# Optimization experiments

Hardware: AMD Instinct MI355X
Metric: run time of the kernel (lower is better)

## Reference

```python
import jax, jax.numpy as jnp
import numpy as np

N_NODES = 50000
N_EDGES = 800000
IN_F, HID, N_CLS = 128, 128, 40


def gcn_conv(x, row, col, ew, W, b, n):
    # PyG GCNConv with add_self_loops=True, normalize=True (gcn_norm):
    # out = D^{-1/2} (A + I) D^{-1/2} (x W) + b, aggregation at target = col.
    h = x @ W                                        # [N, F_out]
    loop = jnp.arange(n)
    row_f = jnp.concatenate([row, loop])             # self-loop weight = 1
    col_f = jnp.concatenate([col, loop])
    ew_f = jnp.concatenate([ew, jnp.ones((n,), dtype=ew.dtype)])
    deg = jax.ops.segment_sum(ew_f, col_f, num_segments=n)
    dinv = jnp.where(deg > 0, jax.lax.rsqrt(deg), 0.0)
    norm = dinv[row_f] * ew_f * dinv[col_f]          # [E+N]
    msg = norm[:, None] * h[row_f]                   # gather + scale
    out = jax.ops.segment_sum(msg, col_f, num_segments=n)  # scatter-add
    return out + b


def setup_inputs() -> dict:
    key = jax.random.key(0)
    ks = jax.random.split(key, 8)
    glorot = lambda k, fi, fo: jax.random.normal(k, (fi, fo), jnp.float32) * np.sqrt(2.0 / (fi + fo))
    return {
        "x": jax.random.normal(ks[0], (N_NODES, IN_F), jnp.float32),
        "edge_weight": jax.random.uniform(ks[1], (N_EDGES,), jnp.float32),
        "W1": glorot(ks[2], IN_F, HID),
        "b1": jnp.zeros((HID,), jnp.float32),
        "W2": glorot(ks[3], HID, HID),
        "b2": jnp.zeros((HID,), jnp.float32),
        "W3": glorot(ks[4], HID, N_CLS),
        "b3": jnp.zeros((N_CLS,), jnp.float32),
        "edge_index": jax.random.randint(ks[5], (2, N_EDGES), 0, N_NODES, jnp.int64),
        "target_mask": jnp.ones((N_NODES,), jnp.bool_),
    }


def reference(x, edge_weight, W1, b1, W2, b2, W3, b3, edge_index, target_mask):
    n = x.shape[0]
    row, col = edge_index[0], edge_index[1]
    h = gcn_conv(x, row, col, edge_weight, W1, b1, n)
    h = jax.nn.relu(h)  # dropout is identity in eval mode
    h = gcn_conv(h, row, col, edge_weight, W2, b2, n)
    h = jax.nn.relu(h)
    h = gcn_conv(h, row, col, edge_weight, W3, b3, n)
    return h[target_mask]
```

## Files before the change

### kernel.cpp

```cpp
#include <hip/hip_runtime.h>
#include <hip/hip_fp16.h>

#define N_NODES 50000
#define N_EDGES 800000
#define HID 128
#define N_CLS 40
#define CAP 64
#define TILES32 1563
#define CNT_BLOCKS 3125
#define NODE_WAVES 12500

static inline int cdiv(int a, int b) { return (a + b - 1) / b; }

__device__ __forceinline__ void fill_body(int e, const int* __restrict__ row,
                                          const int* __restrict__ col,
                                          const float* __restrict__ ew,
                                          int* __restrict__ cnt,
                                          uint2* __restrict__ bkt) {
    if (e < N_EDGES) {
        int c = col[e];
        int pos = atomicAdd(&cnt[c], 1);
        if (pos < CAP)
            bkt[(size_t)c * CAP + pos] = make_uint2((unsigned)row[e],
                                                    __float_as_uint(ew[e]));
    }
}

__device__ __forceinline__ void gemm128_body(int b, const float* __restrict__ X,
                                             const float* __restrict__ W,
                                             __half* __restrict__ out) {
    __shared__ float xsT[128][36];
    __shared__ float wch[32][128];
    const int t = threadIdx.x;
    const int row0 = b * 32;

    #pragma unroll
    for (int i = 0; i < 4; ++i) {
        int idx = t + i * 256;
        int row = idx >> 5;
        int k4  = idx & 31;
        float4 v = make_float4(0.f, 0.f, 0.f, 0.f);
        if (row0 + row < N_NODES)
            v = *(const float4*)&X[(size_t)(row0 + row) * 128 + k4 * 4];
        xsT[k4 * 4 + 0][row] = v.x;
        xsT[k4 * 4 + 1][row] = v.y;
        xsT[k4 * 4 + 2][row] = v.z;
        xsT[k4 * 4 + 3][row] = v.w;
    }

    const int c0 = (t & 31) * 4;
    const int r0 = (t >> 5) * 4;
    float acc[4][4];
    #pragma unroll
    for (int i = 0; i < 4; ++i)
        #pragma unroll
        for (int j = 0; j < 4; ++j) acc[i][j] = 0.f;

    for (int kk = 0; kk < 128; kk += 32) {
        __syncthreads();
        #pragma unroll
        for (int i = 0; i < 4; ++i) {
            int idx = t + i * 256;
            int wr = idx >> 5;
            int wc4 = idx & 31;
            *(float4*)&wch[wr][wc4 * 4] =
                *(const float4*)&W[(size_t)(kk + wr) * 128 + wc4 * 4];
        }
        __syncthreads();
        #pragma unroll 4
        for (int k = 0; k < 32; ++k) {
            float4 a = *(const float4*)&xsT[kk + k][r0];
            float4 w = *(const float4*)&wch[k][c0];
            acc[0][0] = fmaf(a.x, w.x, acc[0][0]);
            acc[0][1] = fmaf(a.x, w.y, acc[0][1]);
            acc[0][2] = fmaf(a.x, w.z, acc[0][2]);
            acc[0][3] = fmaf(a.x, w.w, acc[0][3]);
            acc[1][0] = fmaf(a.y, w.x, acc[1][0]);
            acc[1][1] = fmaf(a.y, w.y, acc[1][1]);
            acc[1][2] = fmaf(a.y, w.z, acc[1][2]);
            acc[1][3] = fmaf(a.y, w.w, acc[1][3]);
            acc[2][0] = fmaf(a.z, w.x, acc[2][0]);
            acc[2][1] = fmaf(a.z, w.y, acc[2][1]);
            acc[2][2] = fmaf(a.z, w.z, acc[2][2]);
            acc[2][3] = fmaf(a.z, w.w, acc[2][3]);
            acc[3][0] = fmaf(a.w, w.x, acc[3][0]);
            acc[3][1] = fmaf(a.w, w.y, acc[3][1]);
            acc[3][2] = fmaf(a.w, w.z, acc[3][2]);
            acc[3][3] = fmaf(a.w, w.w, acc[3][3]);
        }
    }

    #pragma unroll
    for (int i = 0; i < 4; ++i) {
        int r = row0 + r0 + i;
        if (r < N_NODES) {
            union { __half2 h2[2]; float2 f2; } u;
            u.h2[0] = __floats2half2_rn(acc[i][0], acc[i][1]);
            u.h2[1] = __floats2half2_rn(acc[i][2], acc[i][3]);
            *(float2*)&out[(size_t)r * 128 + c0] = u.f2;
        }
    }
}

__global__ __launch_bounds__(256) void fused_gemm1_fill(
    const float* __restrict__ X, const float* __restrict__ W, __half* __restrict__ out,
    const int* __restrict__ row, const int* __restrict__ col,
    const float* __restrict__ ew, int* __restrict__ cnt, uint2* __restrict__ bkt) {
    int id = blockIdx.x;
    if (id & 1) {
        fill_body((id >> 1) * 256 + threadIdx.x, row, col, ew, cnt, bkt);
    } else {
        int b = id >> 1;
        if (b < TILES32) gemm128_body(b, X, W, out);
    }
}

__global__ __launch_bounds__(256) void dinv_kernel(
    const int* __restrict__ cnt, const uint2* __restrict__ bkt,
    float* __restrict__ dinv) {
    int node = blockIdx.x * 4 + (threadIdx.x >> 6);
    int lane = threadIdx.x & 63;
    if (node >= N_NODES) return;
    int n = min(cnt[node], CAP);
    float ewv = 0.f;
    if (lane < n) ewv = __uint_as_float(bkt[(size_t)node * CAP + lane].y);
    #pragma unroll
    for (int off = 32; off > 0; off >>= 1)
        ewv += __shfl_down(ewv, off);
    if (lane == 0) dinv[node] = rsqrtf(ewv + 1.0f);
}

__device__ __forceinline__ void fma_h8(float w, uint4 g, float* acc) {
    float2 a0 = __half22float2(*(const __half2*)&g.x);
    float2 a1 = __half22float2(*(const __half2*)&g.y);
    float2 a2 = __half22float2(*(const __half2*)&g.z);
    float2 a3 = __half22float2(*(const __half2*)&g.w);
    acc[0] = fmaf(w, a0.x, acc[0]);
    acc[1] = fmaf(w, a0.y, acc[1]);
    acc[2] = fmaf(w, a1.x, acc[2]);
    acc[3] = fmaf(w, a1.y, acc[3]);
    acc[4] = fmaf(w, a2.x, acc[4]);
    acc[5] = fmaf(w, a2.y, acc[5]);
    acc[6] = fmaf(w, a3.x, acc[6]);
    acc[7] = fmaf(w, a3.y, acc[7]);
}

__device__ __forceinline__ void agg128_node16(int node, int sl,
                                              const int* __restrict__ cnt,
                                              const uint2* __restrict__ bkt,
                                              const __half* __restrict__ h,
                                              const float* __restrict__ dinv,
                                              const float* __restrict__ bias,
                                              float* acc) {
    #pragma unroll
    for (int j = 0; j < 8; ++j) acc[j] = 0.f;
    if (node >= N_NODES) return;
    int f = sl * 8;
    int beg = node * CAP;
    int end = beg + min(cnt[node], CAP);
    float dn = dinv[node];
    int k = beg;
    for (; k + 8 <= end; k += 8) {
        uint2 e0 = bkt[k],   e1 = bkt[k+1], e2 = bkt[k+2], e3 = bkt[k+3];
        uint2 e4 = bkt[k+4], e5 = bkt[k+5], e6 = bkt[k+6], e7 = bkt[k+7];
        uint4 g0 = *(const uint4*)&h[(size_t)e0.x * 128 + f];
        uint4 g1 = *(const uint4*)&h[(size_t)e1.x * 128 + f];
        uint4 g2 = *(const uint4*)&h[(size_t)e2.x * 128 + f];
        uint4 g3 = *(const uint4*)&h[(size_t)e3.x * 128 + f];
        uint4 g4 = *(const uint4*)&h[(size_t)e4.x * 128 + f];
        uint4 g5 = *(const uint4*)&h[(size_t)e5.x * 128 + f];
        uint4 g6 = *(const uint4*)&h[(size_t)e6.x * 128 + f];
        uint4 g7 = *(const uint4*)&h[(size_t)e7.x * 128 + f];
        float w0 = dinv[e0.x] * __uint_as_float(e0.y) * dn;
        float w1 = dinv[e1.x] * __uint_as_float(e1.y) * dn;
        float w2 = dinv[e2.x] * __uint_as_float(e2.y) * dn;
        float w3 = dinv[e3.x] * __uint_as_float(e3.y) * dn;
        float w4 = dinv[e4.x] * __uint_as_float(e4.y) * dn;
        float w5 = dinv[e5.x] * __uint_as_float(e5.y) * dn;
        float w6 = dinv[e6.x] * __uint_as_float(e6.y) * dn;
        float w7 = dinv[e7.x] * __uint_as_float(e7.y) * dn;
        fma_h8(w0, g0, acc);
        fma_h8(w1, g1, acc);
        fma_h8(w2, g2, acc);
        fma_h8(w3, g3, acc);
        fma_h8(w4, g4, acc);
        fma_h8(w5, g5, acc);
        fma_h8(w6, g6, acc);
        fma_h8(w7, g7, acc);
    }
    for (; k + 4 <= end; k += 4) {
        uint2 e0 = bkt[k], e1 = bkt[k+1], e2 = bkt[k+2], e3 = bkt[k+3];
        uint4 g0 = *(const uint4*)&h[(size_t)e0.x * 128 + f];
        uint4 g1 = *(const uint4*)&h[(size_t)e1.x * 128 + f];
        uint4 g2 = *(const uint4*)&h[(size_t)e2.x * 128 + f];
        uint4 g3 = *(const uint4*)&h[(size_t)e3.x * 128 + f];
        float w0 = dinv[e0.x] * __uint_as_float(e0.y) * dn;
        float w1 = dinv[e1.x] * __uint_as_float(e1.y) * dn;
        float w2 = dinv[e2.x] * __uint_as_float(e2.y) * dn;
        float w3 = dinv[e3.x] * __uint_as_float(e3.y) * dn;
        fma_h8(w0, g0, acc);
        fma_h8(w1, g1, acc);
        fma_h8(w2, g2, acc);
        fma_h8(w3, g3, acc);
    }
    for (; k < end; ++k) {
        uint2 e = bkt[k];
        uint4 g = *(const uint4*)&h[(size_t)e.x * 128 + f];
        float w = dinv[e.x] * __uint_as_float(e.y) * dn;
        fma_h8(w, g, acc);
    }
    uint4 gs = *(const uint4*)&h[(size_t)node * 128 + f];
    fma_h8(dn * dn, gs, acc);
    float4 b0 = *(const float4*)&bias[f];
    float4 b1 = *(const float4*)&bias[f + 4];
    acc[0] = fmaxf(acc[0] + b0.x, 0.f);
    acc[1] = fmaxf(acc[1] + b0.y, 0.f);
    acc[2] = fmaxf(acc[2] + b0.z, 0.f);
    acc[3] = fmaxf(acc[3] + b0.w, 0.f);
    acc[4] = fmaxf(acc[4] + b1.x, 0.f);
    acc[5] = fmaxf(acc[5] + b1.y, 0.f);
    acc[6] = fmaxf(acc[6] + b1.z, 0.f);
    acc[7] = fmaxf(acc[7] + b1.w, 0.f);
}

__device__ __forceinline__ void agg_tile_to_lds(int row0, const int* cnt,
                                                const uint2* bkt, const __half* h,
                                                const float* dinv, const float* bias,
                                                float (*xsT)[36]) {
    int wave = threadIdx.x >> 6;
    int lane = threadIdx.x & 63;
    int sub  = lane >> 4;
    int sl   = lane & 15;
    int f = sl * 8;
    #pragma unroll
    for (int i = 0; i < 2; ++i) {
        int r = i * 16 + wave * 4 + sub;
        float acc[8];
        agg128_node16(row0 + r, sl, cnt, bkt, h, dinv, bias, acc);
        #pragma unroll
        for (int j = 0; j < 8; ++j)
            xsT[f + j][r] = acc[j];
    }
}

__global__ __launch_bounds__(256) void agg_gemm128_kernel(
    const int* __restrict__ cnt, const uint2* __restrict__ bkt,
    const __half* __restrict__ h, const float* __restrict__ dinv,
    const float* __restrict__ bias, const float* __restrict__ W,
    __half* __restrict__ out) {
    __shared__ float xsT[128][36];
    __shared__ float wch[32][128];
    const int t = threadIdx.x;
    const int row0 = blockIdx.x * 32;

    agg_tile_to_lds(row0, cnt, bkt, h, dinv, bias, xsT);

    const int c0 = (t & 31) * 4;
    const int r0 = (t >> 5) * 4;
    float acc[4][4];
    #pragma unroll
    for (int i = 0; i < 4; ++i)
        #pragma unroll
        for (int j = 0; j < 4; ++j) acc[i][j] = 0.f;

    for (int kk = 0; kk < 128; kk += 32) {
        __syncthreads();
        #pragma unroll
        for (int i = 0; i < 4; ++i) {
            int idx = t + i * 256;
            int wr = idx >> 5;
            int wc4 = idx & 31;
            *(float4*)&wch[wr][wc4 * 4] =
                *(const float4*)&W[(size_t)(kk + wr) * 128 + wc4 * 4];
        }
        __syncthreads();
        #pragma unroll 4
        for (int k = 0; k < 32; ++k) {
            float4 a = *(const float4*)&xsT[kk + k][r0];
            float4 w = *(const float4*)&wch[k][c0];
            acc[0][0] = fmaf(a.x, w.x, acc[0][0]);
            acc[0][1] = fmaf(a.x, w.y, acc[0][1]);
            acc[0][2] = fmaf(a.x, w.z, acc[0][2]);
            acc[0][3] = fmaf(a.x, w.w, acc[0][3]);
            acc[1][0] = fmaf(a.y, w.x, acc[1][0]);
            acc[1][1] = fmaf(a.y, w.y, acc[1][1]);
            acc[1][2] = fmaf(a.y, w.z, acc[1][2]);
            acc[1][3] = fmaf(a.y, w.w, acc[1][3]);
            acc[2][0] = fmaf(a.z, w.x, acc[2][0]);
            acc[2][1] = fmaf(a.z, w.y, acc[2][1]);
            acc[2][2] = fmaf(a.z, w.z, acc[2][2]);
            acc[2][3] = fmaf(a.z, w.w, acc[2][3]);
            acc[3][0] = fmaf(a.w, w.x, acc[3][0]);
            acc[3][1] = fmaf(a.w, w.y, acc[3][1]);
            acc[3][2] = fmaf(a.w, w.z, acc[3][2]);
            acc[3][3] = fmaf(a.w, w.w, acc[3][3]);
        }
    }

    #pragma unroll
    for (int i = 0; i < 4; ++i) {
        int r = row0 + r0 + i;
        if (r < N_NODES) {
            union { __half2 h2[2]; float2 f2; } u;
            u.h2[0] = __floats2half2_rn(acc[i][0], acc[i][1]);
            u.h2[1] = __floats2half2_rn(acc[i][2], acc[i][3]);
            *(float2*)&out[(size_t)r * 128 + c0] = u.f2;
        }
    }
}

__global__ __launch_bounds__(256) void agg_gemm40_kernel(
    const int* __restrict__ cnt, const uint2* __restrict__ bkt,
    const __half* __restrict__ h, const float* __restrict__ dinv,
    const float* __restrict__ bias, const float* __restrict__ W3,
    __half* __restrict__ out) {
    __shared__ float xsT[128][36];
    const int row0 = blockIdx.x * 32;
    agg_tile_to_lds(row0, cnt, bkt, h, dinv, bias, xsT);
    __syncthreads();
    for (int idx = threadIdx.x; idx < 32 * N_CLS; idx += 256) {
        int r = idx / N_CLS;
        int c = idx % N_CLS;
        float acc = 0.f;
        #pragma unroll 8
        for (int k = 0; k < 128; ++k)
            acc = fmaf(xsT[k][r], W3[k * N_CLS + c], acc);
        int node = row0 + r;
        if (node < N_NODES)
            out[(size_t)node * 64 + c] = __float2half(acc);
    }
}

__global__ __launch_bounds__(256) void agg40_kernel(
    const int* __restrict__ cnt, const uint2* __restrict__ bkt,
    const __half* __restrict__ h, const float* __restrict__ dinv,
    const float* __restrict__ b, float* __restrict__ out) {
    int wave = threadIdx.x >> 6;
    int lane = threadIdx.x & 63;
    int node = blockIdx.x * 4 + wave;
    if (node >= N_NODES || lane >= N_CLS) return;
    int beg = node * CAP;
    int end = beg + min(cnt[node], CAP);
    float dn = dinv[node];
    float acc = 0.f;
    int k = beg;
    for (; k + 4 <= end; k += 4) {
        uint2 e0 = bkt[k], e1 = bkt[k+1], e2 = bkt[k+2], e3 = bkt[k+3];
        float g0 = __half2float(h[(size_t)e0.x * 64 + lane]);
        float g1 = __half2float(h[(size_t)e1.x * 64 + lane]);
        float g2 = __half2float(h[(size_t)e2.x * 64 + lane]);
        float g3 = __half2float(h[(size_t)e3.x * 64 + lane]);
        float w0 = dinv[e0.x] * __uint_as_float(e0.y) * dn;
        float w1 = dinv[e1.x] * __uint_as_float(e1.y) * dn;
        float w2 = dinv[e2.x] * __uint_as_float(e2.y) * dn;
        float w3 = dinv[e3.x] * __uint_as_float(e3.y) * dn;
        acc = fmaf(w0, g0, acc);
        acc = fmaf(w1, g1, acc);
        acc = fmaf(w2, g2, acc);
        acc = fmaf(w3, g3, acc);
    }
    for (; k < end; ++k) {
        uint2 e = bkt[k];
        float w = dinv[e.x] * __uint_as_float(e.y) * dn;
        acc = fmaf(w, __half2float(h[(size_t)e.x * 64 + lane]), acc);
    }
    acc = fmaf(dn * dn, __half2float(h[(size_t)node * 64 + lane]), acc) + b[lane];
    out[(size_t)node * N_CLS + lane] = acc;
}

extern "C" void kernel_launch(void* const* d_in, const int* in_sizes, int n_in,
                              void* d_out, int out_size, void* d_ws, size_t ws_size,
                              hipStream_t stream) {
    const float* x  = (const float*)d_in[0];
    const float* ew = (const float*)d_in[1];
    const float* W1 = (const float*)d_in[2];
    const float* b1 = (const float*)d_in[3];
    const float* W2 = (const float*)d_in[4];
    const float* b2 = (const float*)d_in[5];
    const float* W3 = (const float*)d_in[6];
    const float* b3 = (const float*)d_in[7];
    const int*   ei = (const int*)d_in[8];
    const int* row = ei;
    const int* col = ei + N_EDGES;
    float* out = (float*)d_out;

    char* ws = (char*)d_ws;
    size_t off = 0;
    auto alloc = [&](size_t bytes) -> void* {
        void* p = (void*)(ws + off);
        off = (off + bytes + 255) & ~(size_t)255;
        return p;
    };
    int*    cnt  = (int*)alloc((size_t)N_NODES * 4);
    float*  dinv = (float*)alloc((size_t)N_NODES * 4);
    uint2*  bkt  = (uint2*)alloc((size_t)N_NODES * CAP * 8);
    __half* h16a = (__half*)alloc((size_t)N_NODES * HID * 2);
    __half* h16b = (__half*)alloc((size_t)N_NODES * HID * 2);
    __half* h40  = (__half*)alloc((size_t)N_NODES * 64 * 2);

    hipMemsetAsync(cnt, 0, (size_t)N_NODES * 4, stream);

    fused_gemm1_fill<<<2 * CNT_BLOCKS, 256, 0, stream>>>(x, W1, h16a, row, col, ew, cnt, bkt);
    dinv_kernel<<<NODE_WAVES, 256, 0, stream>>>(cnt, bkt, dinv);
    agg_gemm128_kernel<<<TILES32, 256, 0, stream>>>(cnt, bkt, h16a, dinv, b1, W2, h16b);
    agg_gemm40_kernel<<<TILES32, 256, 0, stream>>>(cnt, bkt, h16b, dinv, b2, W3, h40);
    agg40_kernel<<<cdiv(N_NODES, 4), 256, 0, stream>>>(cnt, bkt, h40, dinv, b3, out);
}
```

Before: 304.5 us.

## Pack degree sum and count into one 64-bit atomic, drop dinv kernel

The fill step now atomically adds a packed 64-bit value holding the edge count in the high bits and a fixed-point weighted degree in the low 44 bits. This removes the separate dinv reduction kernel and its launch, and the aggregation kernels recompute rsqrt from the packed value on the fly. The trade-offs are 8-byte instead of 4-byte per-neighbor degree loads, an extra rsqrt per edge, and fixed-point rounding of the degree sum. The W2 staging chunk in the agg_gemm128 kernel is also halved to 16 rows, which cuts shared memory but doubles the number of sync steps.

```diff
diff --git a/kernel.cpp b/kernel.cpp
--- a/kernel.cpp
+++ b/kernel.cpp
@@ -8,21 +8,32 @@
 #define CAP 64
 #define TILES32 1563
 #define CNT_BLOCKS 3125
-#define NODE_WAVES 12500
+#define DEG_SCALE 2097152.0f
+#define DEG_MASK ((1ull << 44) - 1)
 
 static inline int cdiv(int a, int b) { return (a + b - 1) / b; }
+
+__device__ __forceinline__ float pdinv(unsigned long long p) {
+    return rsqrtf((float)(p & DEG_MASK) * (1.0f / DEG_SCALE) + 1.0f);
+}
+__device__ __forceinline__ int pcnt(unsigned long long p) {
+    return (int)(p >> 44);
+}
 
 __device__ __forceinline__ void fill_body(int e, const int* __restrict__ row,
                                           const int* __restrict__ col,
                                           const float* __restrict__ ew,
-                                          int* __restrict__ cnt,
+                                          unsigned long long* __restrict__ packed,
                                           uint2* __restrict__ bkt) {
     if (e < N_EDGES) {
         int c = col[e];
-        int pos = atomicAdd(&cnt[c], 1);
+        float w = ew[e];
+        unsigned long long v =
+            (1ull << 44) | (unsigned long long)__float2uint_rn(w * DEG_SCALE);
+        unsigned long long old = atomicAdd(&packed[c], v);
+        int pos = pcnt(old);
         if (pos < CAP)
-            bkt[(size_t)c * CAP + pos] = make_uint2((unsigned)row[e],
-                                                    __float_as_uint(ew[e]));
+            bkt[(size_t)c * CAP + pos] = make_uint2((unsigned)row[e], __float_as_uint(w));
     }
 }
 
@@ -105,29 +116,15 @@
 __global__ __launch_bounds__(256) void fused_gemm1_fill(
     const float* __restrict__ X, const float* __restrict__ W, __half* __restrict__ out,
     const int* __restrict__ row, const int* __restrict__ col,
-    const float* __restrict__ ew, int* __restrict__ cnt, uint2* __restrict__ bkt) {
+    const float* __restrict__ ew, unsigned long long* __restrict__ packed,
+    uint2* __restrict__ bkt) {
     int id = blockIdx.x;
     if (id & 1) {
-        fill_body((id >> 1) * 256 + threadIdx.x, row, col, ew, cnt, bkt);
+        fill_body((id >> 1) * 256 + threadIdx.x, row, col, ew, packed, bkt);
     } else {
         int b = id >> 1;
         if (b < TILES32) gemm128_body(b, X, W, out);
     }
-}
-
-__global__ __launch_bounds__(256) void dinv_kernel(
-    const int* __restrict__ cnt, const uint2* __restrict__ bkt,
-    float* __restrict__ dinv) {
-    int node = blockIdx.x * 4 + (threadIdx.x >> 6);
-    int lane = threadIdx.x & 63;
-    if (node >= N_NODES) return;
-    int n = min(cnt[node], CAP);
-    float ewv = 0.f;
-    if (lane < n) ewv = __uint_as_float(bkt[(size_t)node * CAP + lane].y);
-    #pragma unroll
-    for (int off = 32; off > 0; off >>= 1)
-        ewv += __shfl_down(ewv, off);
-    if (lane == 0) dinv[node] = rsqrtf(ewv + 1.0f);
 }
 
 __device__ __forceinline__ void fma_h8(float w, uint4 g, float* acc) {
@@ -146,19 +143,19 @@
 }
 
 __device__ __forceinline__ void agg128_node16(int node, int sl,
-                                              const int* __restrict__ cnt,
+                                              const unsigned long long* __restrict__ packed,
                                               const uint2* __restrict__ bkt,
                                               const __half* __restrict__ h,
-                                              const float* __restrict__ dinv,
                                               const float* __restrict__ bias,
                                               float* acc) {
     #pragma unroll
     for (int j = 0; j < 8; ++j) acc[j] = 0.f;
     if (node >= N_NODES) return;
     int f = sl * 8;
+    unsigned long long pn = packed[node];
+    float dn = pdinv(pn);
     int beg = node * CAP;
-    int end = beg + min(cnt[node], CAP);
-    float dn = dinv[node];
+    int end = beg + min(pcnt(pn), CAP);
     int k = beg;
     for (; k + 8 <= end; k += 8) {
         uint2 e0 = bkt[k],   e1 = bkt[k+1], e2 = bkt[k+2], e3 = bkt[k+3];
@@ -171,14 +168,14 @@
         uint4 g5 = *(const uint4*)&h[(size_t)e5.x * 128 + f];
         uint4 g6 = *(const uint4*)&h[(size_t)e6.x * 128 + f];
         uint4 g7 = *(const uint4*)&h[(size_t)e7.x * 128 + f];
-        float w0 = dinv[e0.x] * __uint_as_float(e0.y) * dn;
-        float w1 = dinv[e1.x] * __uint_as_float(e1.y) * dn;
-        float w2 = dinv[e2.x] * __uint_as_float(e2.y) * dn;
-        float w3 = dinv[e3.x] * __uint_as_float(e3.y) * dn;
-        float w4 = dinv[e4.x] * __uint_as_float(e4.y) * dn;
-        float w5 = dinv[e5.x] * __uint_as_float(e5.y) * dn;
-        float w6 = dinv[e6.x] * __uint_as_float(e6.y) * dn;
-        float w7 = dinv[e7.x] * __uint_as_float(e7.y) * dn;
+        float w0 = pdinv(packed[e0.x]) * __uint_as_float(e0.y) * dn;
+        float w1 = pdinv(packed[e1.x]) * __uint_as_float(e1.y) * dn;
+        float w2 = pdinv(packed[e2.x]) * __uint_as_float(e2.y) * dn;
+        float w3 = pdinv(packed[e3.x]) * __uint_as_float(e3.y) * dn;
+        float w4 = pdinv(packed[e4.x]) * __uint_as_float(e4.y) * dn;
+        float w5 = pdinv(packed[e5.x]) * __uint_as_float(e5.y) * dn;
+        float w6 = pdinv(packed[e6.x]) * __uint_as_float(e6.y) * dn;
+        float w7 = pdinv(packed[e7.x]) * __uint_as_float(e7.y) * dn;
         fma_h8(w0, g0, acc);
         fma_h8(w1, g1, acc);
         fma_h8(w2, g2, acc);
@@ -194,10 +191,10 @@
         uint4 g1 = *(const uint4*)&h[(size_t)e1.x * 128 + f];
         uint4 g2 = *(const uint4*)&h[(size_t)e2.x * 128 + f];
         uint4 g3 = *(const uint4*)&h[(size_t)e3.x * 128 + f];
-        float w0 = dinv[e0.x] * __uint_as_float(e0.y) * dn;
-        float w1 = dinv[e1.x] * __uint_as_float(e1.y) * dn;
-        float w2 = dinv[e2.x] * __uint_as_float(e2.y) * dn;
-        float w3 = dinv[e3.x] * __uint_as_float(e3.y) * dn;
+        float w0 = pdinv(packed[e0.x]) * __uint_as_float(e0.y) * dn;
+        float w1 = pdinv(packed[e1.x]) * __uint_as_float(e1.y) * dn;
+        float w2 = pdinv(packed[e2.x]) * __uint_as_float(e2.y) * dn;
+        float w3 = pdinv(packed[e3.x]) * __uint_as_float(e3.y) * dn;
         fma_h8(w0, g0, acc);
         fma_h8(w1, g1, acc);
         fma_h8(w2, g2, acc);
@@ -206,7 +203,7 @@
     for (; k < end; ++k) {
         uint2 e = bkt[k];
         uint4 g = *(const uint4*)&h[(size_t)e.x * 128 + f];
-        float w = dinv[e.x] * __uint_as_float(e.y) * dn;
+        float w = pdinv(packed[e.x]) * __uint_as_float(e.y) * dn;
         fma_h8(w, g, acc);
     }
     uint4 gs = *(const uint4*)&h[(size_t)node * 128 + f];
@@ -223,10 +220,10 @@
     acc[7] = fmaxf(acc[7] + b1.w, 0.f);
 }
 
-__device__ __forceinline__ void agg_tile_to_lds(int row0, const int* cnt,
+__device__ __forceinline__ void agg_tile_to_lds(int row0,
+                                                const unsigned long long* packed,
                                                 const uint2* bkt, const __half* h,
-                                                const float* dinv, const float* bias,
-                                                float (*xsT)[36]) {
+                                                const float* bias, float (*xsT)[36]) {
     int wave = threadIdx.x >> 6;
     int lane = threadIdx.x & 63;
     int sub  = lane >> 4;
@@ -236,7 +233,7 @@
     for (int i = 0; i < 2; ++i) {
         int r = i * 16 + wave * 4 + sub;
         float acc[8];
-        agg128_node16(row0 + r, sl, cnt, bkt, h, dinv, bias, acc);
+        agg128_node16(row0 + r, sl, packed, bkt, h, bias, acc);
         #pragma unroll
         for (int j = 0; j < 8; ++j)
             xsT[f + j][r] = acc[j];
@@ -244,16 +241,15 @@
 }
 
 __global__ __launch_bounds__(256) void agg_gemm128_kernel(
-    const int* __restrict__ cnt, const uint2* __restrict__ bkt,
-    const __half* __restrict__ h, const float* __restrict__ dinv,
-    const float* __restrict__ bias, const float* __restrict__ W,
-    __half* __restrict__ out) {
+    const unsigned long long* __restrict__ packed, const uint2* __restrict__ bkt,
+    const __half* __restrict__ h, const float* __restrict__ bias,
+    const float* __restrict__ W, __half* __restrict__ out) {
     __shared__ float xsT[128][36];
-    __shared__ float wch[32][128];
+    __shared__ float wch[16][128];
     const int t = threadIdx.x;
     const int row0 = blockIdx.x * 32;
 
-    agg_tile_to_lds(row0, cnt, bkt, h, dinv, bias, xsT);
+    agg_tile_to_lds(row0, packed, bkt, h, bias, xsT);
 
     const int c0 = (t & 31) * 4;
     const int r0 = (t >> 5) * 4;
@@ -263,10 +259,10 @@
         #pragma unroll
         for (int j = 0; j < 4; ++j) acc[i][j] = 0.f;
 
-    for (int kk = 0; kk < 128; kk += 32) {
+    for (int kk = 0; kk < 128; kk += 16) {
         __syncthreads();
         #pragma unroll
-        for (int i = 0; i < 4; ++i) {
+        for (int i = 0; i < 2; ++i) {
             int idx = t + i * 256;
             int wr = idx >> 5;
             int wc4 = idx & 31;
@@ -275,7 +271,7 @@
         }
         __syncthreads();
         #pragma unroll 4
-        for (int k = 0; k < 32; ++k) {
+        for (int k = 0; k < 16; ++k) {
             float4 a = *(const float4*)&xsT[kk + k][r0];
             float4 w = *(const float4*)&wch[k][c0];
             acc[0][0] = fmaf(a.x, w.x, acc[0][0]);
@@ -310,13 +306,12 @@
 }
 
 __global__ __launch_bounds__(256) void agg_gemm40_kernel(
-    const int* __restrict__ cnt, const uint2* __restrict__ bkt,
-    const __half* __restrict__ h, const float* __restrict__ dinv,
-    const float* __restrict__ bias, const float* __restrict__ W3,
-    __half* __restrict__ out) {
+    const unsigned long long* __restrict__ packed, const uint2* __restrict__ bkt,
+    const __half* __restrict__ h, const float* __restrict__ bias,
+    const float* __restrict__ W3, __half* __restrict__ out) {
     __shared__ float xsT[128][36];
     const int row0 = blockIdx.x * 32;
-    agg_tile_to_lds(row0, cnt, bkt, h, dinv, bias, xsT);
+    agg_tile_to_lds(row0, packed, bkt, h, bias, xsT);
     __syncthreads();
     for (int idx = threadIdx.x; idx < 32 * N_CLS; idx += 256) {
         int r = idx / N_CLS;
@@ -332,16 +327,17 @@
 }
 
 __global__ __launch_bounds__(256) void agg40_kernel(
-    const int* __restrict__ cnt, const uint2* __restrict__ bkt,
-    const __half* __restrict__ h, const float* __restrict__ dinv,
-    const float* __restrict__ b, float* __restrict__ out) {
+    const unsigned long long* __restrict__ packed, const uint2* __restrict__ bkt,
+    const __half* __restrict__ h, const float* __restrict__ b,
+    float* __restrict__ out) {
     int wave = threadIdx.x >> 6;
     int lane = threadIdx.x & 63;
     int node = blockIdx.x * 4 + wave;
     if (node >= N_NODES || lane >= N_CLS) return;
+    unsigned long long pn = packed[node];
+    float dn = pdinv(pn);
     int beg = node * CAP;
-    int end = beg + min(cnt[node], CAP);
-    float dn = dinv[node];
+    int end = beg + min(pcnt(pn), CAP);
     float acc = 0.f;
     int k = beg;
     for (; k + 4 <= end; k += 4) {
@@ -350,10 +346,10 @@
         float g1 = __half2float(h[(size_t)e1.x * 64 + lane]);
         float g2 = __half2float(h[(size_t)e2.x * 64 + lane]);
         float g3 = __half2float(h[(size_t)e3.x * 64 + lane]);
-        float w0 = dinv[e0.x] * __uint_as_float(e0.y) * dn;
-        float w1 = dinv[e1.x] * __uint_as_float(e1.y) * dn;
-        float w2 = dinv[e2.x] * __uint_as_float(e2.y) * dn;
-        float w3 = dinv[e3.x] * __uint_as_float(e3.y) * dn;
+        float w0 = pdinv(packed[e0.x]) * __uint_as_float(e0.y) * dn;
+        float w1 = pdinv(packed[e1.x]) * __uint_as_float(e1.y) * dn;
+        float w2 = pdinv(packed[e2.x]) * __uint_as_float(e2.y) * dn;
+        float w3 = pdinv(packed[e3.x]) * __uint_as_float(e3.y) * dn;
         acc = fmaf(w0, g0, acc);
         acc = fmaf(w1, g1, acc);
         acc = fmaf(w2, g2, acc);
@@ -361,7 +357,7 @@
     }
     for (; k < end; ++k) {
         uint2 e = bkt[k];
-        float w = dinv[e.x] * __uint_as_float(e.y) * dn;
+        float w = pdinv(packed[e.x]) * __uint_as_float(e.y) * dn;
         acc = fmaf(w, __half2float(h[(size_t)e.x * 64 + lane]), acc);
     }
     acc = fmaf(dn * dn, __half2float(h[(size_t)node * 64 + lane]), acc) + b[lane];
@@ -391,18 +387,17 @@
         off = (off + bytes + 255) & ~(size_t)255;
         return p;
     };
-    int*    cnt  = (int*)alloc((size_t)N_NODES * 4);
-    float*  dinv = (float*)alloc((size_t)N_NODES * 4);
+    unsigned long long* packed = (unsigned long long*)alloc((size_t)N_NODES * 8);
     uint2*  bkt  = (uint2*)alloc((size_t)N_NODES * CAP * 8);
     __half* h16a = (__half*)alloc((size_t)N_NODES * HID * 2);
     __half* h16b = (__half*)alloc((size_t)N_NODES * HID * 2);
     __half* h40  = (__half*)alloc((size_t)N_NODES * 64 * 2);
 
-    hipMemsetAsync(cnt, 0, (size_t)N_NODES * 4, stream);
-
-    fused_gemm1_fill<<<2 * CNT_BLOCKS, 256, 0, stream>>>(x, W1, h16a, row, col, ew, cnt, bkt);
-    dinv_kernel<<<NODE_WAVES, 256, 0, stream>>>(cnt, bkt, dinv);
-    agg_gemm128_kernel<<<TILES32, 256, 0, stream>>>(cnt, bkt, h16a, dinv, b1, W2, h16b);
-    agg_gemm40_kernel<<<TILES32, 256, 0, stream>>>(cnt, bkt, h16b, dinv, b2, W3, h40);
-    agg40_kernel<<<cdiv(N_NODES, 4), 256, 0, stream>>>(cnt, bkt, h40, dinv, b3, out);
-}
+    hipMemsetAsync(packed, 0, (size_t)N_NODES * 8, stream);
+
+    fused_gemm1_fill<<<2 * CNT_BLOCKS, 256, 0, stream>>>(x, W1, h16a, row, col, ew,
+                                                         packed, bkt);
+    agg_gemm128_kernel<<<TILES32, 256, 0, stream>>>(packed, bkt, h16a, b1, W2, h16b);
+    agg_gemm40_kernel<<<TILES32, 256, 0, stream>>>(packed, bkt, h16b, b2, W3, h40);
+    agg40_kernel<<<cdiv(N_NODES, 4), 256, 0, stream>>>(packed, bkt, h40, b3, out);
+}
```

Result: slower. 321.6 us (+5.6%).

## Pack edge count and fixed-point degree into one 64-bit atomic

Applied to the files above, without the earlier changes.

The fill pass now uses a single 64-bit atomic per edge that adds both the count (upper bits) and a fixed-point edge weight (lower 44 bits). This lets the degree-normalization kernel become a trivial per-node elementwise pass instead of a wave-per-node reduction over the buckets. The W chunk in the agg_gemm128 kernel is also cut from 32 to 16 rows, which lowers LDS use and may raise occupancy but adds more syncs. The fixed-point degree adds a small quantization error, and 64-bit atomics may cost more than 32-bit ones.

```diff
diff --git a/kernel.cpp b/kernel.cpp
--- a/kernel.cpp
+++ b/kernel.cpp
@@ -8,21 +8,30 @@
 #define CAP 64
 #define TILES32 1563
 #define CNT_BLOCKS 3125
-#define NODE_WAVES 12500
+#define DINV_BLOCKS 196
+#define DEG_SCALE 2097152.0f
+#define DEG_MASK ((1ull << 44) - 1)
 
 static inline int cdiv(int a, int b) { return (a + b - 1) / b; }
+
+__device__ __forceinline__ int pcnt(unsigned long long p) {
+    return (int)(p >> 44);
+}
 
 __device__ __forceinline__ void fill_body(int e, const int* __restrict__ row,
                                           const int* __restrict__ col,
                                           const float* __restrict__ ew,
-                                          int* __restrict__ cnt,
+                                          unsigned long long* __restrict__ packed,
                                           uint2* __restrict__ bkt) {
     if (e < N_EDGES) {
         int c = col[e];
-        int pos = atomicAdd(&cnt[c], 1);
+        float w = ew[e];
+        unsigned long long v =
+            (1ull << 44) | (unsigned long long)__float2uint_rn(w * DEG_SCALE);
+        unsigned long long old = atomicAdd(&packed[c], v);
+        int pos = pcnt(old);
         if (pos < CAP)
-            bkt[(size_t)c * CAP + pos] = make_uint2((unsigned)row[e],
-                                                    __float_as_uint(ew[e]));
+            bkt[(size_t)c * CAP + pos] = make_uint2((unsigned)row[e], __float_as_uint(w));
     }
 }
 
@@ -105,29 +114,22 @@
 __global__ __launch_bounds__(256) void fused_gemm1_fill(
     const float* __restrict__ X, const float* __restrict__ W, __half* __restrict__ out,
     const int* __restrict__ row, const int* __restrict__ col,
-    const float* __restrict__ ew, int* __restrict__ cnt, uint2* __restrict__ bkt) {
+    const float* __restrict__ ew, unsigned long long* __restrict__ packed,
+    uint2* __restrict__ bkt) {
     int id = blockIdx.x;
     if (id & 1) {
-        fill_body((id >> 1) * 256 + threadIdx.x, row, col, ew, cnt, bkt);
+        fill_body((id >> 1) * 256 + threadIdx.x, row, col, ew, packed, bkt);
     } else {
         int b = id >> 1;
         if (b < TILES32) gemm128_body(b, X, W, out);
     }
 }
 
-__global__ __launch_bounds__(256) void dinv_kernel(
-    const int* __restrict__ cnt, const uint2* __restrict__ bkt,
-    float* __restrict__ dinv) {
-    int node = blockIdx.x * 4 + (threadIdx.x >> 6);
-    int lane = threadIdx.x & 63;
-    if (node >= N_NODES) return;
-    int n = min(cnt[node], CAP);
-    float ewv = 0.f;
-    if (lane < n) ewv = __uint_as_float(bkt[(size_t)node * CAP + lane].y);
-    #pragma unroll
-    for (int off = 32; off > 0; off >>= 1)
-        ewv += __shfl_down(ewv, off);
-    if (lane == 0) dinv[node] = rsqrtf(ewv + 1.0f);
+__global__ __launch_bounds__(256) void dinv_from_packed(
+    const unsigned long long* __restrict__ packed, float* __restrict__ dinv) {
+    int i = blockIdx.x * 256 + threadIdx.x;
+    if (i < N_NODES)
+        dinv[i] = rsqrtf((float)(packed[i] & DEG_MASK) * (1.0f / DEG_SCALE) + 1.0f);
 }
 
 __device__ __forceinline__ void fma_h8(float w, uint4 g, float* acc) {
@@ -146,7 +148,7 @@
 }
 
 __device__ __forceinline__ void agg128_node16(int node, int sl,
-                                              const int* __restrict__ cnt,
+                                              const unsigned long long* __restrict__ packed,
                                               const uint2* __restrict__ bkt,
                                               const __half* __restrict__ h,
                                               const float* __restrict__ dinv,
@@ -156,9 +158,9 @@
     for (int j = 0; j < 8; ++j) acc[j] = 0.f;
     if (node >= N_NODES) return;
     int f = sl * 8;
+    float dn = dinv[node];
     int beg = node * CAP;
-    int end = beg + min(cnt[node], CAP);
-    float dn = dinv[node];
+    int end = beg + min(pcnt(packed[node]), CAP);
     int k = beg;
     for (; k + 8 <= end; k += 8) {
         uint2 e0 = bkt[k],   e1 = bkt[k+1], e2 = bkt[k+2], e3 = bkt[k+3];
@@ -223,7 +225,8 @@
     acc[7] = fmaxf(acc[7] + b1.w, 0.f);
 }
 
-__device__ __forceinline__ void agg_tile_to_lds(int row0, const int* cnt,
+__device__ __forceinline__ void agg_tile_to_lds(int row0,
+                                                const unsigned long long* packed,
                                                 const uint2* bkt, const __half* h,
                                                 const float* dinv, const float* bias,
                                                 float (*xsT)[36]) {
@@ -236,7 +239,7 @@
     for (int i = 0; i < 2; ++i) {
         int r = i * 16 + wave * 4 + sub;
         float acc[8];
-        agg128_node16(row0 + r, sl, cnt, bkt, h, dinv, bias, acc);
+        agg128_node16(row0 + r, sl, packed, bkt, h, dinv, bias, acc);
         #pragma unroll
         for (int j = 0; j < 8; ++j)
             xsT[f + j][r] = acc[j];
@@ -244,16 +247,16 @@
 }
 
 __global__ __launch_bounds__(256) void agg_gemm128_kernel(
-    const int* __restrict__ cnt, const uint2* __restrict__ bkt,
+    const unsigned long long* __restrict__ packed, const uint2* __restrict__ bkt,
     const __half* __restrict__ h, const float* __restrict__ dinv,
     const float* __restrict__ bias, const float* __restrict__ W,
     __half* __restrict__ out) {
     __shared__ float xsT[128][36];
-    __shared__ float wch[32][128];
+    __shared__ float wch[16][128];
     const int t = threadIdx.x;
     const int row0 = blockIdx.x * 32;
 
-    agg_tile_to_lds(row0, cnt, bkt, h, dinv, bias, xsT);
+    agg_tile_to_lds(row0, packed, bkt, h, dinv, bias, xsT);
 
     const int c0 = (t & 31) * 4;
     const int r0 = (t >> 5) * 4;
@@ -263,10 +266,10 @@
         #pragma unroll
         for (int j = 0; j < 4; ++j) acc[i][j] = 0.f;
 
-    for (int kk = 0; kk < 128; kk += 32) {
+    for (int kk = 0; kk < 128; kk += 16) {
         __syncthreads();
         #pragma unroll
-        for (int i = 0; i < 4; ++i) {
+        for (int i = 0; i < 2; ++i) {
             int idx = t + i * 256;
             int wr = idx >> 5;
             int wc4 = idx & 31;
@@ -275,7 +278,7 @@
         }
         __syncthreads();
         #pragma unroll 4
-        for (int k = 0; k < 32; ++k) {
+        for (int k = 0; k < 16; ++k) {
             float4 a = *(const float4*)&xsT[kk + k][r0];
             float4 w = *(const float4*)&wch[k][c0];
             acc[0][0] = fmaf(a.x, w.x, acc[0][0]);
@@ -310,13 +313,13 @@
 }
 
 __global__ __launch_bounds__(256) void agg_gemm40_kernel(
-    const int* __restrict__ cnt, const uint2* __restrict__ bkt,
+    const unsigned long long* __restrict__ packed, const uint2* __restrict__ bkt,
     const __half* __restrict__ h, const float* __restrict__ dinv,
     const float* __restrict__ bias, const float* __restrict__ W3,
     __half* __restrict__ out) {
     __shared__ float xsT[128][36];
     const int row0 = blockIdx.x * 32;
-    agg_tile_to_lds(row0, cnt, bkt, h, dinv, bias, xsT);
+    agg_tile_to_lds(row0, packed, bkt, h, dinv, bias, xsT);
     __syncthreads();
     for (int idx = threadIdx.x; idx < 32 * N_CLS; idx += 256) {
         int r = idx / N_CLS;
@@ -332,16 +335,16 @@
 }
 
 __global__ __launch_bounds__(256) void agg40_kernel(
-    const int* __restrict__ cnt, const uint2* __restrict__ bkt,
+    const unsigned long long* __restrict__ packed, const uint2* __restrict__ bkt,
     const __half* __restrict__ h, const float* __restrict__ dinv,
     const float* __restrict__ b, float* __restrict__ out) {
     int wave = threadIdx.x >> 6;
     int lane = threadIdx.x & 63;
     int node = blockIdx.x * 4 + wave;
     if (node >= N_NODES || lane >= N_CLS) return;
+    float dn = dinv[node];
     int beg = node * CAP;
-    int end = beg + min(cnt[node], CAP);
-    float dn = dinv[node];
+    int end = beg + min(pcnt(packed[node]), CAP);
     float acc = 0.f;
     int k = beg;
     for (; k + 4 <= end; k += 4) {
@@ -391,18 +394,19 @@
         off = (off + bytes + 255) & ~(size_t)255;
         return p;
     };
-    int*    cnt  = (int*)alloc((size_t)N_NODES * 4);
+    unsigned long long* packed = (unsigned long long*)alloc((size_t)N_NODES * 8);
     float*  dinv = (float*)alloc((size_t)N_NODES * 4);
     uint2*  bkt  = (uint2*)alloc((size_t)N_NODES * CAP * 8);
     __half* h16a = (__half*)alloc((size_t)N_NODES * HID * 2);
     __half* h16b = (__half*)alloc((size_t)N_NODES * HID * 2);
     __half* h40  = (__half*)alloc((size_t)N_NODES * 64 * 2);
 
-    hipMemsetAsync(cnt, 0, (size_t)N_NODES * 4, stream);
-
-    fused_gemm1_fill<<<2 * CNT_BLOCKS, 256, 0, stream>>>(x, W1, h16a, row, col, ew, cnt, bkt);
-    dinv_kernel<<<NODE_WAVES, 256, 0, stream>>>(cnt, bkt, dinv);
-    agg_gemm128_kernel<<<TILES32, 256, 0, stream>>>(cnt, bkt, h16a, dinv, b1, W2, h16b);
-    agg_gemm40_kernel<<<TILES32, 256, 0, stream>>>(cnt, bkt, h16b, dinv, b2, W3, h40);
-    agg40_kernel<<<cdiv(N_NODES, 4), 256, 0, stream>>>(cnt, bkt, h40, dinv, b3, out);
-}
+    hipMemsetAsync(packed, 0, (size_t)N_NODES * 8, stream);
+
+    fused_gemm1_fill<<<2 * CNT_BLOCKS, 256, 0, stream>>>(x, W1, h16a, row, col, ew,
+                                                         packed, bkt);
+    dinv_from_packed<<<DINV_BLOCKS, 256, 0, stream>>>(packed, dinv);
+    agg_gemm128_kernel<<<TILES32, 256, 0, stream>>>(packed, bkt, h16a, dinv, b1, W2, h16b);
+    agg_gemm40_kernel<<<TILES32, 256, 0, stream>>>(packed, bkt, h16b, dinv, b2, W3, h40);
+    agg40_kernel<<<cdiv(N_NODES, 4), 256, 0, stream>>>(packed, bkt, h40, dinv, b3, out);
+}
```

New measurement: 299.7 us. Within noise of the previous version (-1.6%).
